# Performance work log

Measured on AMD Instinct MI355X. Metric: run time of the kernel, lower is better.

## Reference

```python
import jax, jax.numpy as jnp
import numpy as np

T, B, D_IN, D_H, D_OUT = 128, 256, 256, 1024, 256


def _rand_orth(dim, seed=0):
    rng = np.random.default_rng(seed)
    q, _ = np.linalg.qr(rng.normal(size=(dim, dim)))
    return jnp.asarray(q, dtype=jnp.float32)


def setup_inputs() -> dict:
    key = jax.random.key(0)
    k_xs, k_w1x, k_w2 = jax.random.split(key, 3)
    return {
        "xs": jax.random.normal(k_xs, (T, B, D_IN), dtype=jnp.float32),
        "W1x": 0.1 * jax.random.normal(k_w1x, (D_IN, D_H), dtype=jnp.float32),
        "W1h": _rand_orth(D_H),
        "b1": jnp.zeros((D_H,), dtype=jnp.float32),
        "W2": 0.1 * jax.random.normal(k_w2, (D_H, D_OUT), dtype=jnp.float32),
        "b2": jnp.zeros((), dtype=jnp.float32),
    }


def reference(xs, W1x, W1h, b1, W2, b2):
    # xs: [T, B, D_in]; tanh-RNN recurrence over time, then linear readout.
    h0 = jnp.zeros((xs.shape[1], W1h.shape[0]), dtype=xs.dtype)

    def step(h, x):
        h = jnp.tanh(x @ W1x + h @ W1h + b1)
        return h, None

    h, _ = jax.lax.scan(step, h0, xs)
    return h @ W2 + b2
```

## Files before the change

### kernel.cpp

```cpp
#include <hip/hip_runtime.h>
#include <hip/hip_bf16.h>
#include <math.h>

#define TT   128
#define BB   256
#define DIN  256
#define DH   1024
#define DOUT 256

#define NGM 8
#define MR  32
#define NGN 32
#define NC  32

typedef float  floatx4 __attribute__((ext_vector_type(4)));
typedef short  shortx8 __attribute__((ext_vector_type(8)));
typedef unsigned long long u64;

#define CMASK 0x0001000100010001ULL
#define GSTRIDE 32768

__device__ __forceinline__ short f2bf(float f) {
    union { float f; unsigned u; } v; v.f = f;
    unsigned r = v.u + 0x7fffu + ((v.u >> 16) & 1u);
    return (short)(r >> 16);
}

__device__ __forceinline__ unsigned short bf15e(float v, unsigned bit) {
    union { float f; unsigned u; } x; x.f = v;
    unsigned ua = x.u - (bit << 16);
    unsigned k  = (ua + 0xFFFFu + ((ua >> 17) & 1u)) >> 17;
    return (unsigned short)((k << 1) | bit);
}

__device__ __forceinline__ shortx8 mk8(u64 lo, u64 hi) {
    union { struct { u64 a, b; } s; shortx8 v; } u;
    u.s.a = lo; u.s.b = hi;
    return u.v;
}

__device__ __forceinline__ float fast_tanh(float z) {
    float e = __expf(2.0f * fabsf(z));
    float r = 1.0f - 2.0f / (e + 1.0f);
    return copysignf(r, z);
}

#define AGLD(p)    __hip_atomic_load((p),  __ATOMIC_RELAXED, __HIP_MEMORY_SCOPE_AGENT)
#define AGST(p, v) __hip_atomic_store((p), (v), __ATOMIC_RELAXED, __HIP_MEMORY_SCOPE_AGENT)

#define LD16(buf, base) do { \
    _Pragma("unroll") \
    for (int _j = 0; _j < 8; ++_j) { \
        const u64* _p = (const u64*)(hfr + ((base) + _j) * 512); \
        buf[2 * _j]     = AGLD(_p); \
        buf[2 * _j + 1] = AGLD(_p + 1); \
    } } while (0)
#define OK16(buf, okvar) do { \
    int _o = 1; \
    _Pragma("unroll") \
    for (int _j = 0; _j < 16; ++_j) _o &= ((buf[_j] & CMASK) == pat); \
    okvar = __all(_o); } while (0)
#define WAITVALID(buf, base) do { \
    int _okk; OK16(buf, _okk); \
    while (!_okk) { __builtin_amdgcn_s_sleep(1); LD16(buf, base); OK16(buf, _okk); } \
    } while (0)
#define CONS16(buf, base) do { \
    _Pragma("unroll") \
    for (int _j = 0; _j < 8; ++_j) { \
        shortx8 bfr = mk8(buf[2 * _j], buf[2 * _j + 1]); \
        shortx8 a0 = *(const shortx8*)&WhL[(base) + _j][0][q][lr][0]; \
        shortx8 a1 = *(const shortx8*)&WhL[(base) + _j][1][q][lr][0]; \
        acc0 = __builtin_amdgcn_mfma_f32_16x16x32_bf16(a0, bfr, acc0, 0, 0, 0); \
        acc1 = __builtin_amdgcn_mfma_f32_16x16x32_bf16(a1, bfr, acc1, 0, 0, 0); \
    } } while (0)

__global__ __launch_bounds__(128, 1) void rnn_steps_kernel(
    const float* __restrict__ xs, const float* __restrict__ W1x,
    const float* __restrict__ W1h, const float* __restrict__ b1,
    short* __restrict__ Hbuf)
{
    const int gm  = blockIdx.x;
    const int gn  = blockIdx.y;
    const int tid = threadIdx.x;
    const int w   = tid >> 6;
    const int l   = tid & 63;
    const int lr  = l & 15;
    const int q   = l >> 4;

    const int r0 = gm * MR;
    const int c0 = gn * NC;

    __shared__ short WhL[DH / 32][2][4][16][8];
    for (int idx = tid; idx < (DH / 32) * 2 * 4 * 16; idx += 128) {
        const int c  = idx & 15;
        const int qq = (idx >> 4) & 3;
        const int ct = (idx >> 6) & 1;
        const int ks = idx >> 7;
        shortx8 f;
        #pragma unroll
        for (int j = 0; j < 8; ++j)
            f[j] = f2bf(W1h[(size_t)(ks * 32 + qq * 8 + j) * DH + c0 + ct * 16 + c]);
        *(shortx8*)&WhL[ks][ct][qq][c][0] = f;
    }
    shortx8 wx[2][8];
    #pragma unroll
    for (int ct = 0; ct < 2; ++ct)
        #pragma unroll
        for (int ks = 0; ks < 8; ++ks) {
            shortx8 f;
            #pragma unroll
            for (int j = 0; j < 8; ++j)
                f[j] = f2bf(W1x[(size_t)(ks * 32 + q * 8 + j) * DH + c0 + ct * 16 + lr]);
            wx[ct][ks] = f;
        }
    __syncthreads();

    floatx4 bias[2];
    #pragma unroll
    for (int ct = 0; ct < 2; ++ct)
        #pragma unroll
        for (int r = 0; r < 4; ++r) bias[ct][r] = b1[c0 + ct * 16 + q * 4 + r];

    const int myrow = r0 + w * 16 + lr;
    const size_t HS = (size_t)BB * DH;

    short* const Hg   = Hbuf + gm * GSTRIDE;
    const int rdoff   = w * 16384 + q * 128 + lr * 8;
    const int wroff   = w * 16384 + gn * 512 + (q >> 1) * 128 + lr * 8 + (q & 1) * 4;

    for (int t = 1; t <= TT; ++t) {
        const short* const hfr = Hg + (size_t)((t - 1) & 1) * HS + rdoff;
        const int pc = (t >= 2) ? (1 + ((t - 2) % 15)) : 0;
        const u64 pat = ((u64)(pc & 1)) | ((u64)((pc >> 1) & 1) << 16) |
                        ((u64)((pc >> 2) & 1) << 32) | ((u64)((pc >> 3) & 1) << 48);

        u64 A[16], B[16];
        if (t > 1) LD16(A, 0);

        floatx4 acc0 = {0.f, 0.f, 0.f, 0.f}, acc1 = {0.f, 0.f, 0.f, 0.f};

        {
            const float* xrow = xs + ((size_t)(t - 1) * BB + myrow) * DIN + q * 8;
            #pragma unroll
            for (int ks = 0; ks < 8; ++ks) {
                floatx4 x0 = *(const floatx4*)(xrow + ks * 32);
                floatx4 x1 = *(const floatx4*)(xrow + ks * 32 + 4);
                shortx8 b;
                b[0] = f2bf(x0[0]); b[1] = f2bf(x0[1]); b[2] = f2bf(x0[2]); b[3] = f2bf(x0[3]);
                b[4] = f2bf(x1[0]); b[5] = f2bf(x1[1]); b[6] = f2bf(x1[2]); b[7] = f2bf(x1[3]);
                acc0 = __builtin_amdgcn_mfma_f32_16x16x32_bf16(wx[0][ks], b, acc0, 0, 0, 0);
                acc1 = __builtin_amdgcn_mfma_f32_16x16x32_bf16(wx[1][ks], b, acc1, 0, 0, 0);
            }
        }

        if (t > 1) {
            LD16(B, 8);
            WAITVALID(A, 0);  CONS16(A, 0);
            LD16(A, 16);
            WAITVALID(B, 8);  CONS16(B, 8);
            LD16(B, 24);
            WAITVALID(A, 16); CONS16(A, 16);
            WAITVALID(B, 24); CONS16(B, 24);
        }

        {
            const int cc = 1 + ((t - 1) % 15);
            short* hp = Hg + (size_t)(t & 1) * HS + wroff;
            u64 p0 = 0, p1 = 0;
            #pragma unroll
            for (int r = 0; r < 4; ++r) {
                const unsigned bit = ((unsigned)cc >> r) & 1u;
                p0 |= ((u64)bf15e(fast_tanh(acc0[r] + bias[0][r]), bit)) << (16 * r);
                p1 |= ((u64)bf15e(fast_tanh(acc1[r] + bias[1][r]), bit)) << (16 * r);
            }
            AGST((u64*)(hp), p0);
            AGST((u64*)(hp + 256), p1);
        }
    }
}

__global__ __launch_bounds__(256) void readout_kernel(
    const short* __restrict__ Hfin, const float* __restrict__ W2,
    const float* __restrict__ b2, float* __restrict__ out)
{
    const int o  = threadIdx.x;
    const int b0 = blockIdx.x * 4;
    __shared__ u64 hs8[4 * DH / 4];
    for (int ch = o; ch < 4 * DH / 4; ch += 256) {
        const int row  = ch >> 8;
        const int col0 = (ch & 255) * 4;
        const int rr   = b0 + row;
        const int gmr  = rr >> 5, rt = (rr >> 4) & 1, lrr = rr & 15;
        const int ks   = col0 >> 5, qq = (col0 >> 3) & 3, j0 = col0 & 7;
        const u64* src = (const u64*)(Hfin + (size_t)gmr * GSTRIDE + rt * 16384 +
                                      ks * 512 + qq * 128 + lrr * 8 + j0);
        hs8[ch] = AGLD(src);
    }
    __syncthreads();
    const unsigned* h0 = (const unsigned*)&hs8[0 * 256];
    const unsigned* h1 = (const unsigned*)&hs8[1 * 256];
    const unsigned* h2 = (const unsigned*)&hs8[2 * 256];
    const unsigned* h3 = (const unsigned*)&hs8[3 * 256];
    float a0 = 0.f, a1 = 0.f, a2 = 0.f, a3 = 0.f;
    for (int k2 = 0; k2 < DH / 2; ++k2) {
        float w0 = W2[(2 * k2)     * DOUT + o];
        float w1 = W2[(2 * k2 + 1) * DOUT + o];
        unsigned p0 = h0[k2], p1 = h1[k2], p2 = h2[k2], p3 = h3[k2];
        a0 += __builtin_bit_cast(float, p0 << 16) * w0 + __builtin_bit_cast(float, p0 & 0xffff0000u) * w1;
        a1 += __builtin_bit_cast(float, p1 << 16) * w0 + __builtin_bit_cast(float, p1 & 0xffff0000u) * w1;
        a2 += __builtin_bit_cast(float, p2 << 16) * w0 + __builtin_bit_cast(float, p2 & 0xffff0000u) * w1;
        a3 += __builtin_bit_cast(float, p3 << 16) * w0 + __builtin_bit_cast(float, p3 & 0xffff0000u) * w1;
    }
    const float bias = b2[0];
    out[(b0 + 0) * DOUT + o] = a0 + bias;
    out[(b0 + 1) * DOUT + o] = a1 + bias;
    out[(b0 + 2) * DOUT + o] = a2 + bias;
    out[(b0 + 3) * DOUT + o] = a3 + bias;
}

extern "C" void kernel_launch(void* const* d_in, const int* in_sizes, int n_in,
                              void* d_out, int out_size, void* d_ws, size_t ws_size,
                              hipStream_t stream) {
    (void)in_sizes; (void)n_in; (void)out_size; (void)ws_size;
    const float* xs  = (const float*)d_in[0];
    const float* W1x = (const float*)d_in[1];
    const float* W1h = (const float*)d_in[2];
    const float* b1  = (const float*)d_in[3];
    const float* W2  = (const float*)d_in[4];
    const float* b2  = (const float*)d_in[5];
    float* out = (float*)d_out;

    short* Hbuf = (short*)d_ws;

    rnn_steps_kernel<<<dim3(NGM, NGN), 128, 0, stream>>>(xs, W1x, W1h, b1, Hbuf);
    readout_kernel<<<dim3(BB / 4), 256, 0, stream>>>(Hbuf, W2, b2, out);
}
```

Baseline: 753.8 us.

## Use multi-slot ring buffer for hidden state and issue all loads upfront

When the workspace is large enough, hidden states go into a 63-slot ring buffer instead of a double buffer. All four 16-chunk groups of the previous state are then fetched up front with plain vector loads instead of interleaved relaxed atomic loads. The validity check on the chunk pattern is still applied before each group is consumed. The goal is to issue loads earlier and remove atomic-load overhead, but it depends on ws_size and needs a larger memory footprint.

After: 979.0 us. 1.3x slower.

```diff
diff --git a/kernel.cpp b/kernel.cpp
--- a/kernel.cpp
+++ b/kernel.cpp
@@ -54,6 +54,13 @@
         const u64* _p = (const u64*)(hfr + ((base) + _j) * 512); \
         buf[2 * _j]     = AGLD(_p); \
         buf[2 * _j + 1] = AGLD(_p + 1); \
+    } } while (0)
+#define LD16P(buf, base) do { \
+    _Pragma("unroll") \
+    for (int _j = 0; _j < 8; ++_j) { \
+        union { shortx8 s; u64 d[2]; } _u; \
+        _u.s = *(const shortx8*)(hfr + ((base) + _j) * 512); \
+        buf[2 * _j] = _u.d[0]; buf[2 * _j + 1] = _u.d[1]; \
     } } while (0)
 #define OK16(buf, okvar) do { \
     int _o = 1; \
@@ -77,7 +84,7 @@
 __global__ __launch_bounds__(128, 1) void rnn_steps_kernel(
     const float* __restrict__ xs, const float* __restrict__ W1x,
     const float* __restrict__ W1h, const float* __restrict__ b1,
-    short* __restrict__ Hbuf)
+    short* __restrict__ Hbuf, int big, int M)
 {
     const int gm  = blockIdx.x;
     const int gn  = blockIdx.y;
@@ -124,18 +131,26 @@
     const int myrow = r0 + w * 16 + lr;
     const size_t HS = (size_t)BB * DH;
 
-    short* const Hg   = Hbuf + gm * GSTRIDE;
-    const int rdoff   = w * 16384 + q * 128 + lr * 8;
-    const int wroff   = w * 16384 + gn * 512 + (q >> 1) * 128 + lr * 8 + (q & 1) * 4;
+    short* const Hg = Hbuf + gm * GSTRIDE;
+    const int rdoff = w * 16384 + q * 128 + lr * 8;
+    const int wroff = w * 16384 + gn * 512 + (q >> 1) * 128 + lr * 8 + (q & 1) * 4;
+
+    int cv = 1 % M, pv = 0;
 
     for (int t = 1; t <= TT; ++t) {
-        const short* const hfr = Hg + (size_t)((t - 1) & 1) * HS + rdoff;
+        const short* const hfr = Hg + (size_t)pv * HS + rdoff;
         const int pc = (t >= 2) ? (1 + ((t - 2) % 15)) : 0;
         const u64 pat = ((u64)(pc & 1)) | ((u64)((pc >> 1) & 1) << 16) |
                         ((u64)((pc >> 2) & 1) << 32) | ((u64)((pc >> 3) & 1) << 48);
 
-        u64 A[16], B[16];
-        if (t > 1) LD16(A, 0);
+        u64 A[16], B[16], C[16], D[16];
+        if (t > 1) {
+            if (big) {
+                LD16P(A, 0); LD16P(B, 8); LD16P(C, 16); LD16P(D, 24);
+            } else {
+                LD16(A, 0);
+            }
+        }
 
         floatx4 acc0 = {0.f, 0.f, 0.f, 0.f}, acc1 = {0.f, 0.f, 0.f, 0.f};
 
@@ -154,18 +169,25 @@
         }
 
         if (t > 1) {
-            LD16(B, 8);
-            WAITVALID(A, 0);  CONS16(A, 0);
-            LD16(A, 16);
-            WAITVALID(B, 8);  CONS16(B, 8);
-            LD16(B, 24);
-            WAITVALID(A, 16); CONS16(A, 16);
-            WAITVALID(B, 24); CONS16(B, 24);
+            if (big) {
+                WAITVALID(A, 0);  CONS16(A, 0);
+                WAITVALID(B, 8);  CONS16(B, 8);
+                WAITVALID(C, 16); CONS16(C, 16);
+                WAITVALID(D, 24); CONS16(D, 24);
+            } else {
+                LD16(B, 8);
+                WAITVALID(A, 0);  CONS16(A, 0);
+                LD16(C, 16);
+                WAITVALID(B, 8);  CONS16(B, 8);
+                LD16(D, 24);
+                WAITVALID(C, 16); CONS16(C, 16);
+                WAITVALID(D, 24); CONS16(D, 24);
+            }
         }
 
         {
             const int cc = 1 + ((t - 1) % 15);
-            short* hp = Hg + (size_t)(t & 1) * HS + wroff;
+            short* hp = Hg + (size_t)cv * HS + wroff;
             u64 p0 = 0, p1 = 0;
             #pragma unroll
             for (int r = 0; r < 4; ++r) {
@@ -176,6 +198,8 @@
             AGST((u64*)(hp), p0);
             AGST((u64*)(hp + 256), p1);
         }
+
+        pv = cv; cv = (cv + 1 == M) ? 0 : cv + 1;
     }
 }
 
@@ -221,7 +245,7 @@
 extern "C" void kernel_launch(void* const* d_in, const int* in_sizes, int n_in,
                               void* d_out, int out_size, void* d_ws, size_t ws_size,
                               hipStream_t stream) {
-    (void)in_sizes; (void)n_in; (void)out_size; (void)ws_size;
+    (void)in_sizes; (void)n_in; (void)out_size;
     const float* xs  = (const float*)d_in[0];
     const float* W1x = (const float*)d_in[1];
     const float* W1h = (const float*)d_in[2];
@@ -230,8 +254,13 @@
     const float* b2  = (const float*)d_in[5];
     float* out = (float*)d_out;
 
+    const size_t HS = (size_t)BB * DH;
+    int M = 63, big = 1;
+    if (ws_size < (size_t)63 * HS * sizeof(short) + 1024) { big = 0; M = 2; }
     short* Hbuf = (short*)d_ws;
 
-    rnn_steps_kernel<<<dim3(NGM, NGN), 128, 0, stream>>>(xs, W1x, W1h, b1, Hbuf);
-    readout_kernel<<<dim3(BB / 4), 256, 0, stream>>>(Hbuf, W2, b2, out);
-}
+    rnn_steps_kernel<<<dim3(NGM, NGN), 128, 0, stream>>>(
+        xs, W1x, W1h, b1, Hbuf, big, M);
+    const short* Hfin = Hbuf + (size_t)(TT % M) * HS;
+    readout_kernel<<<dim3(BB / 4), 256, 0, stream>>>(Hfin, W2, b2, out);
+}
```

## Widen per-block hidden tile to 64 columns using 128KB dynamic LDS

Applied to the files above, without the earlier changes.

Adds a variant of the persistent RNN step kernel in which each block owns 64 hidden columns instead of 32. This halves the grid to 128 blocks, and each block keeps a 128KB bf16 slice of W1h in dynamic shared memory. Every h fragment loaded from global memory now feeds four MFMA chains instead of two, so fewer blocks take part in the per-step flag-polling synchronisation and the global h traffic per FLOP drops. In exchange each step has a longer serial MFMA chain per block and half as many CUs are used. The launcher falls back to the old 32-column kernel if the large shared-memory attribute cannot be set.

After: 1.255 ms. 66.5% more time.

```diff
diff --git a/kernel.cpp b/kernel.cpp
--- a/kernel.cpp
+++ b/kernel.cpp
@@ -9,9 +9,6 @@
 #define DOUT 256
 
 #define NGM 8
-#define MR  32
-#define NGN 32
-#define NC  32
 
 typedef float  floatx4 __attribute__((ext_vector_type(4)));
 typedef short  shortx8 __attribute__((ext_vector_type(8)));
@@ -64,17 +61,8 @@
     int _okk; OK16(buf, _okk); \
     while (!_okk) { __builtin_amdgcn_s_sleep(1); LD16(buf, base); OK16(buf, _okk); } \
     } while (0)
-#define CONS16(buf, base) do { \
-    _Pragma("unroll") \
-    for (int _j = 0; _j < 8; ++_j) { \
-        shortx8 bfr = mk8(buf[2 * _j], buf[2 * _j + 1]); \
-        shortx8 a0 = *(const shortx8*)&WhL[(base) + _j][0][q][lr][0]; \
-        shortx8 a1 = *(const shortx8*)&WhL[(base) + _j][1][q][lr][0]; \
-        acc0 = __builtin_amdgcn_mfma_f32_16x16x32_bf16(a0, bfr, acc0, 0, 0, 0); \
-        acc1 = __builtin_amdgcn_mfma_f32_16x16x32_bf16(a1, bfr, acc1, 0, 0, 0); \
-    } } while (0)
-
-__global__ __launch_bounds__(128, 1) void rnn_steps_kernel(
+
+__global__ __launch_bounds__(128, 1) void rnn_steps_kernel64(
     const float* __restrict__ xs, const float* __restrict__ W1x,
     const float* __restrict__ W1h, const float* __restrict__ b1,
     short* __restrict__ Hbuf)
@@ -87,8 +75,130 @@
     const int lr  = l & 15;
     const int q   = l >> 4;
 
-    const int r0 = gm * MR;
-    const int c0 = gn * NC;
+    const int r0 = gm * 32;
+    const int c0 = gn * 64;
+
+    extern __shared__ short WhL[];
+    for (int idx = tid; idx < 8192; idx += 128) {
+        const int c  = idx & 15;
+        const int qq = (idx >> 4) & 3;
+        const int ct = (idx >> 6) & 3;
+        const int ks = idx >> 8;
+        shortx8 f;
+        #pragma unroll
+        for (int j = 0; j < 8; ++j)
+            f[j] = f2bf(W1h[(size_t)(ks * 32 + qq * 8 + j) * DH + c0 + ct * 16 + c]);
+        *(shortx8*)&WhL[(size_t)(((ks * 4 + ct) * 4 + qq) * 16 + c) * 8] = f;
+    }
+    shortx8 wx[4][8];
+    #pragma unroll
+    for (int ct = 0; ct < 4; ++ct)
+        #pragma unroll
+        for (int ks = 0; ks < 8; ++ks) {
+            shortx8 f;
+            #pragma unroll
+            for (int j = 0; j < 8; ++j)
+                f[j] = f2bf(W1x[(size_t)(ks * 32 + q * 8 + j) * DH + c0 + ct * 16 + lr]);
+            wx[ct][ks] = f;
+        }
+    __syncthreads();
+
+    floatx4 bias[4];
+    #pragma unroll
+    for (int ct = 0; ct < 4; ++ct)
+        #pragma unroll
+        for (int r = 0; r < 4; ++r) bias[ct][r] = b1[c0 + ct * 16 + q * 4 + r];
+
+    const int myrow = r0 + w * 16 + lr;
+    const size_t HS = (size_t)BB * DH;
+    short* const Hg = Hbuf + gm * GSTRIDE;
+    const int rdoff = w * 16384 + q * 128 + lr * 8;
+    int wroff[4];
+    #pragma unroll
+    for (int ct = 0; ct < 4; ++ct)
+        wroff[ct] = w * 16384 + (gn * 2 + (ct >> 1)) * 512 +
+                    ((ct & 1) * 2 + (q >> 1)) * 128 + lr * 8 + (q & 1) * 4;
+
+    for (int t = 1; t <= TT; ++t) {
+        const short* const hfr = Hg + (size_t)((t - 1) & 1) * HS + rdoff;
+        const int pc = (t >= 2) ? (1 + ((t - 2) % 15)) : 0;
+        const u64 pat = ((u64)(pc & 1)) | ((u64)((pc >> 1) & 1) << 16) |
+                        ((u64)((pc >> 2) & 1) << 32) | ((u64)((pc >> 3) & 1) << 48);
+
+        u64 A[16], B[16];
+        if (t > 1) LD16(A, 0);
+
+        floatx4 acc[4] = {{0,0,0,0},{0,0,0,0},{0,0,0,0},{0,0,0,0}};
+
+        {
+            const float* xrow = xs + ((size_t)(t - 1) * BB + myrow) * DIN + q * 8;
+            #pragma unroll
+            for (int ks = 0; ks < 8; ++ks) {
+                floatx4 x0 = *(const floatx4*)(xrow + ks * 32);
+                floatx4 x1 = *(const floatx4*)(xrow + ks * 32 + 4);
+                shortx8 b;
+                b[0] = f2bf(x0[0]); b[1] = f2bf(x0[1]); b[2] = f2bf(x0[2]); b[3] = f2bf(x0[3]);
+                b[4] = f2bf(x1[0]); b[5] = f2bf(x1[1]); b[6] = f2bf(x1[2]); b[7] = f2bf(x1[3]);
+                #pragma unroll
+                for (int ct = 0; ct < 4; ++ct)
+                    acc[ct] = __builtin_amdgcn_mfma_f32_16x16x32_bf16(wx[ct][ks], b, acc[ct], 0, 0, 0);
+            }
+        }
+
+        if (t > 1) {
+            #define CONS16_4(buf, base) do { \
+                _Pragma("unroll") \
+                for (int _j = 0; _j < 8; ++_j) { \
+                    shortx8 bfr = mk8(buf[2 * _j], buf[2 * _j + 1]); \
+                    _Pragma("unroll") \
+                    for (int _ct = 0; _ct < 4; ++_ct) { \
+                        const shortx8 a = *(const shortx8*)&WhL[ \
+                            (size_t)(((((base) + _j) * 4 + _ct) * 4 + q) * 16 + lr) * 8]; \
+                        acc[_ct] = __builtin_amdgcn_mfma_f32_16x16x32_bf16(a, bfr, acc[_ct], 0, 0, 0); \
+                    } \
+                } } while (0)
+            LD16(B, 8);
+            WAITVALID(A, 0);  CONS16_4(A, 0);
+            LD16(A, 16);
+            WAITVALID(B, 8);  CONS16_4(B, 8);
+            LD16(B, 24);
+            WAITVALID(A, 16); CONS16_4(A, 16);
+            WAITVALID(B, 24); CONS16_4(B, 24);
+            #undef CONS16_4
+        }
+
+        {
+            const int cc = 1 + ((t - 1) % 15);
+            short* hv = Hg + (size_t)(t & 1) * HS;
+            #pragma unroll
+            for (int ct = 0; ct < 4; ++ct) {
+                u64 p = 0;
+                #pragma unroll
+                for (int r = 0; r < 4; ++r) {
+                    const unsigned bit = ((unsigned)cc >> r) & 1u;
+                    p |= ((u64)bf15e(fast_tanh(acc[ct][r] + bias[ct][r]), bit)) << (16 * r);
+                }
+                AGST((u64*)(hv + wroff[ct]), p);
+            }
+        }
+    }
+}
+
+__global__ __launch_bounds__(128, 1) void rnn_steps_kernel32(
+    const float* __restrict__ xs, const float* __restrict__ W1x,
+    const float* __restrict__ W1h, const float* __restrict__ b1,
+    short* __restrict__ Hbuf)
+{
+    const int gm  = blockIdx.x;
+    const int gn  = blockIdx.y;
+    const int tid = threadIdx.x;
+    const int w   = tid >> 6;
+    const int l   = tid & 63;
+    const int lr  = l & 15;
+    const int q   = l >> 4;
+
+    const int r0 = gm * 32;
+    const int c0 = gn * 32;
 
     __shared__ short WhL[DH / 32][2][4][16][8];
     for (int idx = tid; idx < (DH / 32) * 2 * 4 * 16; idx += 128) {
@@ -123,10 +233,9 @@
 
     const int myrow = r0 + w * 16 + lr;
     const size_t HS = (size_t)BB * DH;
-
-    short* const Hg   = Hbuf + gm * GSTRIDE;
-    const int rdoff   = w * 16384 + q * 128 + lr * 8;
-    const int wroff   = w * 16384 + gn * 512 + (q >> 1) * 128 + lr * 8 + (q & 1) * 4;
+    short* const Hg = Hbuf + gm * GSTRIDE;
+    const int rdoff = w * 16384 + q * 128 + lr * 8;
+    const int wroff = w * 16384 + gn * 512 + (q >> 1) * 128 + lr * 8 + (q & 1) * 4;
 
     for (int t = 1; t <= TT; ++t) {
         const short* const hfr = Hg + (size_t)((t - 1) & 1) * HS + rdoff;
@@ -138,7 +247,6 @@
         if (t > 1) LD16(A, 0);
 
         floatx4 acc0 = {0.f, 0.f, 0.f, 0.f}, acc1 = {0.f, 0.f, 0.f, 0.f};
-
         {
             const float* xrow = xs + ((size_t)(t - 1) * BB + myrow) * DIN + q * 8;
             #pragma unroll
@@ -152,17 +260,25 @@
                 acc1 = __builtin_amdgcn_mfma_f32_16x16x32_bf16(wx[1][ks], b, acc1, 0, 0, 0);
             }
         }
-
         if (t > 1) {
+            #define CONS16_2(buf, base) do { \
+                _Pragma("unroll") \
+                for (int _j = 0; _j < 8; ++_j) { \
+                    shortx8 bfr = mk8(buf[2 * _j], buf[2 * _j + 1]); \
+                    shortx8 a0 = *(const shortx8*)&WhL[(base) + _j][0][q][lr][0]; \
+                    shortx8 a1 = *(const shortx8*)&WhL[(base) + _j][1][q][lr][0]; \
+                    acc0 = __builtin_amdgcn_mfma_f32_16x16x32_bf16(a0, bfr, acc0, 0, 0, 0); \
+                    acc1 = __builtin_amdgcn_mfma_f32_16x16x32_bf16(a1, bfr, acc1, 0, 0, 0); \
+                } } while (0)
             LD16(B, 8);
-            WAITVALID(A, 0);  CONS16(A, 0);
+            WAITVALID(A, 0);  CONS16_2(A, 0);
             LD16(A, 16);
-            WAITVALID(B, 8);  CONS16(B, 8);
+            WAITVALID(B, 8);  CONS16_2(B, 8);
             LD16(B, 24);
-            WAITVALID(A, 16); CONS16(A, 16);
-            WAITVALID(B, 24); CONS16(B, 24);
-        }
-
+            WAITVALID(A, 16); CONS16_2(A, 16);
+            WAITVALID(B, 24); CONS16_2(B, 24);
+            #undef CONS16_2
+        }
         {
             const int cc = 1 + ((t - 1) % 15);
             short* hp = Hg + (size_t)(t & 1) * HS + wroff;
@@ -232,6 +348,15 @@
 
     short* Hbuf = (short*)d_ws;
 
-    rnn_steps_kernel<<<dim3(NGM, NGN), 128, 0, stream>>>(xs, W1x, W1h, b1, Hbuf);
+    hipError_t e = hipFuncSetAttribute(
+        reinterpret_cast<const void*>(rnn_steps_kernel64),
+        hipFuncAttributeMaxDynamicSharedMemorySize, 131072);
+    if (e == hipSuccess) {
+        rnn_steps_kernel64<<<dim3(NGM, 16), 128, 131072, stream>>>(
+            xs, W1x, W1h, b1, Hbuf);
+    } else {
+        rnn_steps_kernel32<<<dim3(NGM, 32), 128, 0, stream>>>(
+            xs, W1x, W1h, b1, Hbuf);
+    }
     readout_kernel<<<dim3(BB / 4), 256, 0, stream>>>(Hbuf, W2, b2, out);
 }
```
